# Optimization experiments

Measured on AMD Instinct MI355X. Metric: run time of the kernel, lower is better.

The kernel has to match this reference:

```python
import jax, jax.numpy as jnp
import numpy as np

B, C, H, W = 8, 256, 64, 64
CK = C // 8  # query/key channels


def setup_inputs() -> dict:
    key = jax.random.key(0)
    ks = jax.random.split(key, 8)
    s = 1.0 / np.sqrt(C)
    return {
        "x": jax.random.normal(ks[0], (B, C, H, W), dtype=jnp.float32),
        "Wq": jax.random.normal(ks[1], (CK, C), dtype=jnp.float32) * s,
        "bq": jax.random.normal(ks[2], (CK,), dtype=jnp.float32) * 0.01,
        "Wk": jax.random.normal(ks[3], (CK, C), dtype=jnp.float32) * s,
        "bk": jax.random.normal(ks[4], (CK,), dtype=jnp.float32) * 0.01,
        "Wv": jax.random.normal(ks[5], (C, C), dtype=jnp.float32) * s,
        "bv": jax.random.normal(ks[6], (C,), dtype=jnp.float32) * 0.01,
        "gamma": jax.random.normal(ks[7], (1,), dtype=jnp.float32) * 0.1,
    }


def reference(x, Wq, bq, Wk, bk, Wv, bv, gamma):
    b, c, h, w = x.shape
    n = h * w
    xf = x.reshape(b, c, n)                       # [B,C,N]
    # 1x1 convs == channel-wise linear maps
    q = jnp.einsum('oc,bcn->bon', Wq, xf) + bq[:, None]   # [B,CK,N]
    k = jnp.einsum('oc,bcn->bon', Wk, xf) + bk[:, None]   # [B,CK,N]
    v = jnp.einsum('oc,bcn->bon', Wv, xf) + bv[:, None]   # [B,C,N]
    energy = jnp.einsum('bcm,bcn->bmn', q, k)             # [B,N,N] (query rows m)
    attn = jax.nn.softmax(energy, axis=-1)
    out = jnp.einsum('bcn,bmn->bcm', v, attn)             # value @ attn^T
    out = out.reshape(b, c, h, w)
    return gamma * out + x
```

## Files before the change

kernel.cpp:

```cpp
#include <hip/hip_runtime.h>
#include <stdint.h>

typedef unsigned short u16;
typedef unsigned int u32;
typedef __bf16 bf16_t;
typedef __bf16 bf16x4 __attribute__((ext_vector_type(4)));
typedef __bf16 bf16x8 __attribute__((ext_vector_type(8)));
typedef float f32x4 __attribute__((ext_vector_type(4)));
typedef float f32x16 __attribute__((ext_vector_type(16)));

#define LOG2E 1.4426950408889634f
#define MFMA32(a, b, c) __builtin_amdgcn_mfma_f32_32x32x16_bf16(a, b, c, 0, 0, 0)

__device__ __forceinline__ u16 f2bf(float f) {
    union { float f; unsigned int u; } v; v.f = f;
    unsigned int r = v.u + 0x7fffu + ((v.u >> 16) & 1u);
    return (u16)(r >> 16);
}

__device__ __forceinline__ bf16x8 ld8f_bf(const float* __restrict__ p) {
    float4 a = *reinterpret_cast<const float4*>(p);
    float4 b = *reinterpret_cast<const float4*>(p + 4);
    bf16x8 r;
    r[0] = (bf16_t)a.x; r[1] = (bf16_t)a.y; r[2] = (bf16_t)a.z; r[3] = (bf16_t)a.w;
    r[4] = (bf16_t)b.x; r[5] = (bf16_t)b.y; r[6] = (bf16_t)b.z; r[7] = (bf16_t)b.w;
    return r;
}

__device__ __forceinline__ u32 cvt_pk_bf16(float a, float b) {
    u32 r;
    asm("v_cvt_pk_bf16_f32 %0, %1, %2" : "=v"(r) : "v"(a), "v"(b));
    return r;
}

__device__ __forceinline__ void plane32_swap(u32& a, u32& b) {
    asm("v_permlane32_swap_b32 %0, %1" : "+v"(a), "+v"(b));
}

__device__ __forceinline__ bf16x8 pack8(const float* p) {
    u32 c0 = cvt_pk_bf16(p[0], p[1]);
    u32 c1 = cvt_pk_bf16(p[2], p[3]);
    u32 c2 = cvt_pk_bf16(p[4], p[5]);
    u32 c3 = cvt_pk_bf16(p[6], p[7]);
    plane32_swap(c0, c2);
    plane32_swap(c1, c3);
    union { u32 u[4]; bf16x8 v; } f;
    f.u[0] = c0; f.u[1] = c1; f.u[2] = c2; f.u[3] = c3;
    return f.v;
}

__device__ __forceinline__ void g2lds16(const u16* g, u16* l) {
    __builtin_amdgcn_global_load_lds(
        (const __attribute__((address_space(1))) unsigned int*)g,
        (__attribute__((address_space(3))) unsigned int*)l, 16, 0, 0);
}

__global__ __launch_bounds__(256) void k_transpose(
    const float* __restrict__ x,
    const float* __restrict__ Wq, const float* __restrict__ Wk,
    const float* __restrict__ Wv,
    u16* __restrict__ xT, u16* __restrict__ wqkb, u16* __restrict__ wvb) {
    int blk = blockIdx.x;
    int t = threadIdx.x;
    if (blk >= 2048) {
        if (blk == 2048) {
            for (int j = 0; j < 8; ++j) {
                int fg = j * 256 + t;
                int n = fg >> 5, g = fg & 31;
                const float* src = (n < 32) ? (Wq + (size_t)n * 256 + g * 8)
                                            : (Wk + (size_t)(n - 32) * 256 + g * 8);
                *reinterpret_cast<bf16x8*>(wqkb + n * 256 + ((g ^ (n & 7)) << 3)) =
                    ld8f_bf(src);
            }
        } else {
            int base = (blk - 2049) * 2048;
            for (int j = 0; j < 8; ++j) {
                int fg = base + j * 256 + t;
                int slice = fg >> 10, d = fg & 1023;
                int co = d >> 2, g2 = (d & 3) ^ (co & 3);
                *reinterpret_cast<bf16x8*>(wvb + fg * 8) =
                    ld8f_bf(Wv + (size_t)co * 256 + slice * 32 + g2 * 8);
            }
        }
        return;
    }
    __shared__ u16 tile[64][68];
    int b = blk >> 8;
    int r = blk & 255;
    int c0 = (r & 3) * 64;
    int n0 = (r >> 2) * 64;
    const float* xb = x + (size_t)b * 256 * 4096;
    u16* xTb = xT + (size_t)b * 4096 * 256;
    int lc = t >> 4;
    int l4 = (t & 15) * 4;
    #pragma unroll
    for (int p = 0; p < 4; ++p) {
        int c = lc + p * 16;
        float4 v = *reinterpret_cast<const float4*>(xb + (size_t)(c0 + c) * 4096 + n0 + l4);
        tile[c][l4 + 0] = f2bf(v.x); tile[c][l4 + 1] = f2bf(v.y);
        tile[c][l4 + 2] = f2bf(v.z); tile[c][l4 + 3] = f2bf(v.w);
    }
    __syncthreads();
    #pragma unroll
    for (int p = 0; p < 4; ++p) {
        int n = lc + p * 16;
        ushort4 v;
        v.x = tile[l4 + 0][n]; v.y = tile[l4 + 1][n];
        v.z = tile[l4 + 2][n]; v.w = tile[l4 + 3][n];
        int gslot = ((c0 + l4) >> 3) ^ ((n0 + n) & 7);
        *reinterpret_cast<ushort4*>(
            xTb + (size_t)(n0 + n) * 256 + (gslot << 3) + (l4 & 7)) = v;
    }
}

__global__ __launch_bounds__(512, 2) void k_proj(
    const u16* __restrict__ xT, const u16* __restrict__ wqkb,
    const u16* __restrict__ wvb,
    const float* __restrict__ bq, const float* __restrict__ bk,
    const float* __restrict__ bv,
    u16* __restrict__ qt, u16* __restrict__ kt, u16* __restrict__ vt) {
    __shared__ u16 Xs[128 * 256];
    __shared__ u16 Ws[64 * 256];
    __shared__ u16 Wvs[256 * 32];
    int blk = blockIdx.x;
    int b = blk & 7;
    int n0 = (blk >> 3) * 128;
    int t = threadIdx.x;
    int w = t >> 6;
    int lane = t & 63;
    int lo = lane & 15;
    int q = lane >> 4;
    const u16* xTb = xT + (size_t)b * 4096 * 256;

    #pragma unroll
    for (int p = 0; p < 8; ++p)
        g2lds16(xTb + (size_t)n0 * 256 + (p * 512 + t) * 8, &Xs[(p * 512 + w * 64) * 8]);
    #pragma unroll
    for (int p = 0; p < 4; ++p)
        g2lds16(wqkb + (p * 512 + t) * 8, &Ws[(p * 512 + w * 64) * 8]);

    f32x4 accqk[4] = {};
    f32x4 accv[16];
    #pragma unroll
    for (int i = 0; i < 16; ++i) accv[i] = f32x4{0.f, 0.f, 0.f, 0.f};

    int rowA = w * 16 + lo;
    int cw = (w & 3) * 64;
    int nh = (w >> 2) * 64;
    for (int c0 = 0; c0 < 256; c0 += 32) {
        __syncthreads();
        #pragma unroll
        for (int p = 0; p < 2; ++p)
            g2lds16(wvb + (size_t)(c0 >> 5) * 8192 + (p * 512 + t) * 8,
                    &Wvs[(p * 512 + w * 64) * 8]);
        __syncthreads();

        int K = c0 >> 3;
        bf16x8 a = *reinterpret_cast<const bf16x8*>(
            &Xs[(rowA * 32 + ((K + q) ^ (lo & 7))) * 8]);
        #pragma unroll
        for (int ot = 0; ot < 4; ++ot) {
            bf16x8 bb = *reinterpret_cast<const bf16x8*>(
                &Ws[((ot * 16 + lo) * 32 + ((K + q) ^ (lo & 7))) * 8]);
            accqk[ot] = __builtin_amdgcn_mfma_f32_16x16x32_bf16(a, bb, accqk[ot], 0, 0, 0);
        }
        bf16x8 xbf[4];
        #pragma unroll
        for (int nt = 0; nt < 4; ++nt)
            xbf[nt] = *reinterpret_cast<const bf16x8*>(
                &Xs[((nh + nt * 16 + lo) * 32 + ((K + q) ^ (lo & 7))) * 8]);
        #pragma unroll
        for (int ct = 0; ct < 4; ++ct) {
            int co = cw + ct * 16 + lo;
            bf16x8 av = *reinterpret_cast<const bf16x8*>(
                &Wvs[(co * 4 + (q ^ (co & 3))) * 8]);
            #pragma unroll
            for (int nt = 0; nt < 4; ++nt)
                accv[ct * 4 + nt] = __builtin_amdgcn_mfma_f32_16x16x32_bf16(
                    av, xbf[nt], accv[ct * 4 + nt], 0, 0, 0);
        }
    }
    #pragma unroll
    for (int ot = 0; ot < 4; ++ot) {
        float bias = (ot < 2) ? bq[ot * 16 + lo] : bk[(ot - 2) * 16 + lo];
        #pragma unroll
        for (int r = 0; r < 4; ++r) {
            int n = n0 + w * 16 + q * 4 + r;
            float val = accqk[ot][r] + bias;
            if (ot < 2) qt[((size_t)b * 4096 + n) * 32 + ot * 16 + lo] = f2bf(val * LOG2E);
            else        kt[((size_t)b * 4096 + n) * 32 + (ot - 2) * 16 + lo] = f2bf(val);
        }
    }
    #pragma unroll
    for (int ct = 0; ct < 4; ++ct) {
        #pragma unroll
        for (int nt = 0; nt < 4; ++nt) {
            int nt_g = ((n0 + nh) >> 4) + nt;
            #pragma unroll
            for (int r = 0; r < 4; ++r) {
                int co = cw + ct * 16 + q * 4 + r;
                float val = accv[ct * 4 + nt][r] + bv[co];
                vt[(((size_t)b * 256 + nt_g) * 256 + co) * 16 + lo] = f2bf(val);
            }
        }
    }
}

#define FLASH_PV_A(FC0, FC1, Vc_)                                              \
    {                                                                          \
        bf16x8 v0_ = *reinterpret_cast<const bf16x8*>(Vc_ + gslot8);           \
        bf16x8 v1_ = *reinterpret_cast<const bf16x8*>(Vc_ + 512 + gslot8);     \
        bf16x8 v2_ = *reinterpret_cast<const bf16x8*>(Vc_ + 1024 + gslot8);    \
        bf16x8 v3_ = *reinterpret_cast<const bf16x8*>(Vc_ + 1536 + gslot8);    \
        __builtin_amdgcn_s_setprio(1);                                         \
        O0 = MFMA32(v0_, FC0, O0); O1 = MFMA32(v1_, FC0, O1);                  \
        O0 = MFMA32(v2_, FC1, O0); O1 = MFMA32(v3_, FC1, O1);                  \
        __builtin_amdgcn_s_setprio(0);                                         \
    }

#define FLASH_PV_B(FC2, FC3, Vc_)                                              \
    {                                                                          \
        bf16x8 v0_ = *reinterpret_cast<const bf16x8*>(Vc_ + 2048 + gslot8);    \
        bf16x8 v1_ = *reinterpret_cast<const bf16x8*>(Vc_ + 2560 + gslot8);    \
        bf16x8 v2_ = *reinterpret_cast<const bf16x8*>(Vc_ + 3072 + gslot8);    \
        bf16x8 v3_ = *reinterpret_cast<const bf16x8*>(Vc_ + 3584 + gslot8);    \
        __builtin_amdgcn_s_setprio(1);                                         \
        O0 = MFMA32(v0_, FC2, O0); O1 = MFMA32(v1_, FC2, O1);                  \
        O0 = MFMA32(v2_, FC3, O0); O1 = MFMA32(v3_, FC3, O1);                  \
        __builtin_amdgcn_s_setprio(0);                                         \
    }

#define FLASH_ITER(S_, VDN)                                                    \
    {                                                                          \
        const int s_ = (S_);                                                   \
        const u16* Vc_ = Vs[s_ & 1];                                           \
        float p_[8];                                                           \
        bf16x8 f0_, f1_;                                                       \
        {                                                                      \
            f32x16 St_ = MFMA32(kC0, qf0, z16);                                \
            St_ = MFMA32(kC1, qf1, St_);                                       \
            _Pragma("unroll")                                                  \
            for (int i_ = 0; i_ < 8; ++i_) {                                   \
                p_[i_] = __builtin_amdgcn_exp2f(St_[i_]); lsum += p_[i_];      \
            }                                                                  \
            f0_ = pack8(p_);                                                   \
            _Pragma("unroll")                                                  \
            for (int i_ = 0; i_ < 8; ++i_) {                                   \
                p_[i_] = __builtin_amdgcn_exp2f(St_[8 + i_]); lsum += p_[i_];  \
            }                                                                  \
            f1_ = pack8(p_);                                                   \
        }                                                                      \
        FLASH_PV_A(f0_, f1_, Vc_)                                              \
        {                                                                      \
            f32x16 St_ = MFMA32(kC2, qf0, z16);                                \
            St_ = MFMA32(kC3, qf1, St_);                                       \
            const u16* kp_ = kbase + (size_t)(((s_ + 1) & 63) * 2048);         \
            kC0 = *reinterpret_cast<const bf16x8*>(kp_);                       \
            kC1 = *reinterpret_cast<const bf16x8*>(kp_ + 16);                  \
            kC2 = *reinterpret_cast<const bf16x8*>(kp_ + 1024);                \
            kC3 = *reinterpret_cast<const bf16x8*>(kp_ + 1040);                \
            const u16* vs_ = vstage + (size_t)(((s_ + 1) & 63)) * 16384;       \
            g2lds16(vs_,       VDN);                                           \
            g2lds16(vs_ + 512, VDN + 512);                                     \
            _Pragma("unroll")                                                  \
            for (int i_ = 0; i_ < 8; ++i_) {                                   \
                p_[i_] = __builtin_amdgcn_exp2f(St_[i_]); lsum += p_[i_];      \
            }                                                                  \
            f0_ = pack8(p_);                                                   \
            _Pragma("unroll")                                                  \
            for (int i_ = 0; i_ < 8; ++i_) {                                   \
                p_[i_] = __builtin_amdgcn_exp2f(St_[8 + i_]); lsum += p_[i_];  \
            }                                                                  \
            f1_ = pack8(p_);                                                   \
        }                                                                      \
        FLASH_PV_B(f0_, f1_, Vc_)                                              \
        __syncthreads();                                                       \
    }

__global__ __launch_bounds__(256, 4) void k_flash(
    const u16* __restrict__ qt, const u16* __restrict__ kt,
    const u16* __restrict__ vt, const float* __restrict__ x,
    const float* __restrict__ gamma, float* __restrict__ out) {
    __shared__ u16 Vs[2][4096];
    int blk = blockIdx.x;
    int b = blk & 7;
    int rest = blk >> 3;
    int m0 = (rest & 31) * 128;
    int ch0 = (rest >> 5) * 64;
    int t = threadIdx.x;
    int w = t >> 6;
    int lane = t & 63;
    int la = lane & 31;
    int hi = lane >> 5;

    const u16* qtb = qt + (size_t)b * 4096 * 32;
    const u16* ktb = kt + (size_t)b * 4096 * 32;
    const u16* vtb = vt + (size_t)b * 256 * 256 * 16;

    int qw0 = m0 + w * 32;
    bf16x8 qf0 = *reinterpret_cast<const bf16x8*>(qtb + (size_t)(qw0 + la) * 32 + hi * 8);
    bf16x8 qf1 = *reinterpret_cast<const bf16x8*>(qtb + (size_t)(qw0 + la) * 32 + 16 + hi * 8);

    const u16* kbase = ktb + (size_t)la * 32 + hi * 8;

    int g = la * 2 + hi;
    int gslot8 = (g ^ (g >> 3)) * 8;
    int sg = lane ^ (lane >> 3);
    const u16* vstage = vtb + ((size_t)(w * 256) + ch0) * 16 + sg * 8;
    u16* vd0 = &Vs[0][w * 1024];
    u16* vd1 = &Vs[1][w * 1024];

    f32x16 O0 = {}, O1 = {};
    const f32x16 z16 = {};
    float lsum = 0.f;

    bf16x8 kC0, kC1, kC2, kC3;

    kC0 = *reinterpret_cast<const bf16x8*>(kbase);
    kC1 = *reinterpret_cast<const bf16x8*>(kbase + 16);
    kC2 = *reinterpret_cast<const bf16x8*>(kbase + 1024);
    kC3 = *reinterpret_cast<const bf16x8*>(kbase + 1040);
    g2lds16(vstage,       vd0);
    g2lds16(vstage + 512, vd0 + 512);
    __syncthreads();

    for (int ss = 0; ss < 32; ++ss) {
        int s0 = ss * 2;
        FLASH_ITER(s0,     vd1)
        FLASH_ITER(s0 + 1, vd0)
    }

    lsum += __shfl_xor(lsum, 32, 64);
    float linv = 1.0f / lsum;
    float gm = gamma[0];
    const float* xb = x + (size_t)b * 256 * 4096;
    float* ob = out + (size_t)b * 256 * 4096;
    int m = m0 + w * 32 + la;
    #pragma unroll
    for (int r = 0; r < 16; ++r) {
        int crow = (r & 3) + 8 * (r >> 2) + 4 * hi;
        size_t i0 = (size_t)(ch0 + crow) * 4096 + m;
        ob[i0]             = gm * (O0[r] * linv) + xb[i0];
        ob[i0 + 32 * 4096] = gm * (O1[r] * linv) + xb[i0 + 32 * 4096];
    }
}

extern "C" void kernel_launch(void* const* d_in, const int* in_sizes, int n_in,
                              void* d_out, int out_size, void* d_ws, size_t ws_size,
                              hipStream_t stream) {
    const float* x     = (const float*)d_in[0];
    const float* Wq    = (const float*)d_in[1];
    const float* bq    = (const float*)d_in[2];
    const float* Wk    = (const float*)d_in[3];
    const float* bk    = (const float*)d_in[4];
    const float* Wv    = (const float*)d_in[5];
    const float* bv    = (const float*)d_in[6];
    const float* gamma = (const float*)d_in[7];
    float* out = (float*)d_out;

    char* ws = (char*)d_ws;
    u16* xT   = (u16*)d_out;
    u16* wqkb = (u16*)d_out + 8388608;
    u16* wvb  = (u16*)d_out + 8388608 + 16384;
    u16* qt = (u16*)ws;
    u16* kt = (u16*)(ws + 2097152);
    u16* vt = (u16*)(ws + 2 * 2097152);

    k_transpose<<<2053, 256, 0, stream>>>(x, Wq, Wk, Wv, xT, wqkb, wvb);
    k_proj<<<256, 512, 0, stream>>>(xT, wqkb, wvb, bq, bk, bv, qt, kt, vt);
    k_flash<<<1024, 256, 0, stream>>>(qt, kt, vt, x, gamma, out);
}
```

Baseline: 237.2 us.

## Widen flash tile to 128 channels and split keys across two wave groups

Measured after the change: 324.3 us. 1.37x slower.

```diff
diff --git a/kernel.cpp b/kernel.cpp
--- a/kernel.cpp
+++ b/kernel.cpp
@@ -206,7 +206,7 @@
     }
 }
 
-#define FLASH_PV_A(FC0, FC1, Vc_)                                              \
+#define FLASH_PV_HALF1(FC0, FC1, Vc_)                                          \
     {                                                                          \
         bf16x8 v0_ = *reinterpret_cast<const bf16x8*>(Vc_ + gslot8);           \
         bf16x8 v1_ = *reinterpret_cast<const bf16x8*>(Vc_ + 512 + gslot8);     \
@@ -214,26 +214,42 @@
         bf16x8 v3_ = *reinterpret_cast<const bf16x8*>(Vc_ + 1536 + gslot8);    \
         __builtin_amdgcn_s_setprio(1);                                         \
         O0 = MFMA32(v0_, FC0, O0); O1 = MFMA32(v1_, FC0, O1);                  \
-        O0 = MFMA32(v2_, FC1, O0); O1 = MFMA32(v3_, FC1, O1);                  \
+        O2 = MFMA32(v2_, FC0, O2); O3 = MFMA32(v3_, FC0, O3);                  \
         __builtin_amdgcn_s_setprio(0);                                         \
-    }
-
-#define FLASH_PV_B(FC2, FC3, Vc_)                                              \
+        bf16x8 v4_ = *reinterpret_cast<const bf16x8*>(Vc_ + 2048 + gslot8);    \
+        bf16x8 v5_ = *reinterpret_cast<const bf16x8*>(Vc_ + 2560 + gslot8);    \
+        bf16x8 v6_ = *reinterpret_cast<const bf16x8*>(Vc_ + 3072 + gslot8);    \
+        bf16x8 v7_ = *reinterpret_cast<const bf16x8*>(Vc_ + 3584 + gslot8);    \
+        __builtin_amdgcn_s_setprio(1);                                         \
+        O0 = MFMA32(v4_, FC1, O0); O1 = MFMA32(v5_, FC1, O1);                  \
+        O2 = MFMA32(v6_, FC1, O2); O3 = MFMA32(v7_, FC1, O3);                  \
+        __builtin_amdgcn_s_setprio(0);                                         \
+    }
+
+#define FLASH_PV_HALF2(FC2, FC3, Vc_)                                          \
     {                                                                          \
-        bf16x8 v0_ = *reinterpret_cast<const bf16x8*>(Vc_ + 2048 + gslot8);    \
-        bf16x8 v1_ = *reinterpret_cast<const bf16x8*>(Vc_ + 2560 + gslot8);    \
-        bf16x8 v2_ = *reinterpret_cast<const bf16x8*>(Vc_ + 3072 + gslot8);    \
-        bf16x8 v3_ = *reinterpret_cast<const bf16x8*>(Vc_ + 3584 + gslot8);    \
+        bf16x8 v0_ = *reinterpret_cast<const bf16x8*>(Vc_ + 4096 + gslot8);    \
+        bf16x8 v1_ = *reinterpret_cast<const bf16x8*>(Vc_ + 4608 + gslot8);    \
+        bf16x8 v2_ = *reinterpret_cast<const bf16x8*>(Vc_ + 5120 + gslot8);    \
+        bf16x8 v3_ = *reinterpret_cast<const bf16x8*>(Vc_ + 5632 + gslot8);    \
         __builtin_amdgcn_s_setprio(1);                                         \
         O0 = MFMA32(v0_, FC2, O0); O1 = MFMA32(v1_, FC2, O1);                  \
-        O0 = MFMA32(v2_, FC3, O0); O1 = MFMA32(v3_, FC3, O1);                  \
+        O2 = MFMA32(v2_, FC2, O2); O3 = MFMA32(v3_, FC2, O3);                  \
+        __builtin_amdgcn_s_setprio(0);                                         \
+        bf16x8 v4_ = *reinterpret_cast<const bf16x8*>(Vc_ + 6144 + gslot8);    \
+        bf16x8 v5_ = *reinterpret_cast<const bf16x8*>(Vc_ + 6656 + gslot8);    \
+        bf16x8 v6_ = *reinterpret_cast<const bf16x8*>(Vc_ + 7168 + gslot8);    \
+        bf16x8 v7_ = *reinterpret_cast<const bf16x8*>(Vc_ + 7680 + gslot8);    \
+        __builtin_amdgcn_s_setprio(1);                                         \
+        O0 = MFMA32(v4_, FC3, O0); O1 = MFMA32(v5_, FC3, O1);                  \
+        O2 = MFMA32(v6_, FC3, O2); O3 = MFMA32(v7_, FC3, O3);                  \
         __builtin_amdgcn_s_setprio(0);                                         \
     }
 
 #define FLASH_ITER(S_, VDN)                                                    \
     {                                                                          \
         const int s_ = (S_);                                                   \
-        const u16* Vc_ = Vs[s_ & 1];                                           \
+        const u16* Vc_ = Vs_my + (size_t)((s_ & 1) * 8192);                    \
         float p_[8];                                                           \
         bf16x8 f0_, f1_;                                                       \
         {                                                                      \
@@ -250,18 +266,20 @@
             }                                                                  \
             f1_ = pack8(p_);                                                   \
         }                                                                      \
-        FLASH_PV_A(f0_, f1_, Vc_)                                              \
+        FLASH_PV_HALF1(f0_, f1_, Vc_)                                          \
         {                                                                      \
             f32x16 St_ = MFMA32(kC2, qf0, z16);                                \
             St_ = MFMA32(kC3, qf1, St_);                                       \
-            const u16* kp_ = kbase + (size_t)(((s_ + 1) & 63) * 2048);         \
+            const u16* kp_ = kbase + (size_t)(((s_ + 1) & 31) * 2048);         \
             kC0 = *reinterpret_cast<const bf16x8*>(kp_);                       \
             kC1 = *reinterpret_cast<const bf16x8*>(kp_ + 16);                  \
             kC2 = *reinterpret_cast<const bf16x8*>(kp_ + 1024);                \
             kC3 = *reinterpret_cast<const bf16x8*>(kp_ + 1040);                \
-            const u16* vs_ = vstage + (size_t)(((s_ + 1) & 63)) * 16384;       \
-            g2lds16(vs_,       VDN);                                           \
-            g2lds16(vs_ + 512, VDN + 512);                                     \
+            const u16* vs_ = vstage + (size_t)(((s_ + 1) & 31)) * 16384;       \
+            g2lds16(vs_,        VDN);                                          \
+            g2lds16(vs_ + 512,  VDN + 512);                                    \
+            g2lds16(vs_ + 1024, VDN + 1024);                                   \
+            g2lds16(vs_ + 1536, VDN + 1536);                                   \
             _Pragma("unroll")                                                  \
             for (int i_ = 0; i_ < 8; ++i_) {                                   \
                 p_[i_] = __builtin_amdgcn_exp2f(St_[i_]); lsum += p_[i_];      \
@@ -273,22 +291,25 @@
             }                                                                  \
             f1_ = pack8(p_);                                                   \
         }                                                                      \
-        FLASH_PV_B(f0_, f1_, Vc_)                                              \
+        FLASH_PV_HALF2(f0_, f1_, Vc_)                                          \
         __syncthreads();                                                       \
     }
 
-__global__ __launch_bounds__(256, 4) void k_flash(
+__global__ __launch_bounds__(512, 4) void k_flash(
     const u16* __restrict__ qt, const u16* __restrict__ kt,
     const u16* __restrict__ vt, const float* __restrict__ x,
     const float* __restrict__ gamma, float* __restrict__ out) {
-    __shared__ u16 Vs[2][4096];
+    __shared__ u16 Vs[2][2][8192];
+    __shared__ float Ls[4][32];
     int blk = blockIdx.x;
     int b = blk & 7;
     int rest = blk >> 3;
     int m0 = (rest & 31) * 128;
-    int ch0 = (rest >> 5) * 64;
+    int ch0 = (rest >> 5) * 128;
     int t = threadIdx.x;
     int w = t >> 6;
+    int qw = w & 3;
+    int kh = w >> 2;
     int lane = t & 63;
     int la = lane & 31;
     int hi = lane >> 5;
@@ -297,20 +318,21 @@
     const u16* ktb = kt + (size_t)b * 4096 * 32;
     const u16* vtb = vt + (size_t)b * 256 * 256 * 16;
 
-    int qw0 = m0 + w * 32;
+    int qw0 = m0 + qw * 32;
     bf16x8 qf0 = *reinterpret_cast<const bf16x8*>(qtb + (size_t)(qw0 + la) * 32 + hi * 8);
     bf16x8 qf1 = *reinterpret_cast<const bf16x8*>(qtb + (size_t)(qw0 + la) * 32 + 16 + hi * 8);
 
-    const u16* kbase = ktb + (size_t)la * 32 + hi * 8;
+    const u16* kbase = ktb + (size_t)(kh * 2048 + la) * 32 + hi * 8;
 
     int g = la * 2 + hi;
     int gslot8 = (g ^ (g >> 3)) * 8;
     int sg = lane ^ (lane >> 3);
-    const u16* vstage = vtb + ((size_t)(w * 256) + ch0) * 16 + sg * 8;
-    u16* vd0 = &Vs[0][w * 1024];
-    u16* vd1 = &Vs[1][w * 1024];
-
-    f32x16 O0 = {}, O1 = {};
+    const u16* vstage = vtb + ((size_t)((kh * 128 + qw) * 256) + ch0) * 16 + sg * 8;
+    u16* Vs_my = &Vs[kh][0][0];
+    u16* vd0 = Vs_my + qw * 2048;
+    u16* vd1 = Vs_my + 8192 + qw * 2048;
+
+    f32x16 O0 = {}, O1 = {}, O2 = {}, O3 = {};
     const f32x16 z16 = {};
     float lsum = 0.f;
 
@@ -320,28 +342,56 @@
     kC1 = *reinterpret_cast<const bf16x8*>(kbase + 16);
     kC2 = *reinterpret_cast<const bf16x8*>(kbase + 1024);
     kC3 = *reinterpret_cast<const bf16x8*>(kbase + 1040);
-    g2lds16(vstage,       vd0);
-    g2lds16(vstage + 512, vd0 + 512);
+    g2lds16(vstage,        vd0);
+    g2lds16(vstage + 512,  vd0 + 512);
+    g2lds16(vstage + 1024, vd0 + 1024);
+    g2lds16(vstage + 1536, vd0 + 1536);
     __syncthreads();
 
-    for (int ss = 0; ss < 32; ++ss) {
+    for (int ss = 0; ss < 16; ++ss) {
         int s0 = ss * 2;
         FLASH_ITER(s0,     vd1)
         FLASH_ITER(s0 + 1, vd0)
     }
 
     lsum += __shfl_xor(lsum, 32, 64);
-    float linv = 1.0f / lsum;
-    float gm = gamma[0];
-    const float* xb = x + (size_t)b * 256 * 4096;
-    float* ob = out + (size_t)b * 256 * 4096;
-    int m = m0 + w * 32 + la;
-    #pragma unroll
-    for (int r = 0; r < 16; ++r) {
-        int crow = (r & 3) + 8 * (r >> 2) + 4 * hi;
-        size_t i0 = (size_t)(ch0 + crow) * 4096 + m;
-        ob[i0]             = gm * (O0[r] * linv) + xb[i0];
-        ob[i0 + 32 * 4096] = gm * (O1[r] * linv) + xb[i0 + 32 * 4096];
+
+    float* Cmb = (float*)&Vs[0][0][0];
+    int cbase = qw * 4096 + lane;
+    if (kh == 1) {
+        if (lane < 32) Ls[qw][lane] = lsum;
+        #pragma unroll
+        for (int r = 0; r < 16; ++r) {
+            Cmb[cbase + (0 * 16 + r) * 64] = O0[r];
+            Cmb[cbase + (1 * 16 + r) * 64] = O1[r];
+            Cmb[cbase + (2 * 16 + r) * 64] = O2[r];
+            Cmb[cbase + (3 * 16 + r) * 64] = O3[r];
+        }
+    }
+    __syncthreads();
+    if (kh == 0) {
+        lsum += Ls[qw][la];
+        #pragma unroll
+        for (int r = 0; r < 16; ++r) {
+            O0[r] += Cmb[cbase + (0 * 16 + r) * 64];
+            O1[r] += Cmb[cbase + (1 * 16 + r) * 64];
+            O2[r] += Cmb[cbase + (2 * 16 + r) * 64];
+            O3[r] += Cmb[cbase + (3 * 16 + r) * 64];
+        }
+        float linv = 1.0f / lsum;
+        float gm = gamma[0];
+        const float* xb = x + (size_t)b * 256 * 4096;
+        float* ob = out + (size_t)b * 256 * 4096;
+        int m = m0 + qw * 32 + la;
+        #pragma unroll
+        for (int r = 0; r < 16; ++r) {
+            int crow = (r & 3) + 8 * (r >> 2) + 4 * hi;
+            size_t i0 = (size_t)(ch0 + crow) * 4096 + m;
+            ob[i0]             = gm * (O0[r] * linv) + xb[i0];
+            ob[i0 + 32 * 4096] = gm * (O1[r] * linv) + xb[i0 + 32 * 4096];
+            ob[i0 + 64 * 4096] = gm * (O2[r] * linv) + xb[i0 + 64 * 4096];
+            ob[i0 + 96 * 4096] = gm * (O3[r] * linv) + xb[i0 + 96 * 4096];
+        }
     }
 }
 
@@ -368,5 +418,5 @@
 
     k_transpose<<<2053, 256, 0, stream>>>(x, Wq, Wk, Wv, xT, wqkb, wvb);
     k_proj<<<256, 512, 0, stream>>>(xT, wqkb, wvb, bq, bk, bv, qt, kt, vt);
-    k_flash<<<1024, 256, 0, stream>>>(qt, kt, vt, x, gamma, out);
-}
+    k_flash<<<512, 512, 0, stream>>>(qt, kt, vt, x, gamma, out);
+}
```
